# Optimization experiments

Hardware: AMD Instinct MI355X
Metric: run time of the kernel (lower is better)

## Reference

```python
import jax, jax.numpy as jnp
import numpy as np

KH, KW = 3, 3
STRIDE, PAD = 2, 1
NEG_SLOPE = 0.2
EPS = 1e-5


def conv2d(x, w, stride, pad):
    return jax.lax.conv_general_dilated(
        x, w, window_strides=(stride, stride),
        padding=[(pad, pad), (pad, pad)],
        dimension_numbers=('NCHW', 'OIHW', 'NCHW'))


def deform_conv2d(x, offsets, w_def):
    # x: [B,C,H,W]; offsets: [B,2*K,Ho,Wo] (per-kernel-tap (dy,dx) pairs);
    # w_def: [Cout,Cin,KH,KW]. Matches torchvision DeformConv2d (v1, no mask).
    B, C, H, W = x.shape
    Ho, Wo = offsets.shape[2], offsets.shape[3]
    K = KH * KW
    off = offsets.reshape(B, K, 2, Ho, Wo)
    dy, dx = off[:, :, 0], off[:, :, 1]            # [B,K,Ho,Wo]

    ky = jnp.arange(KH).repeat(KW).astype(x.dtype)   # [K]
    kx = jnp.tile(jnp.arange(KW), KH).astype(x.dtype)
    base_y = (jnp.arange(Ho) * STRIDE - PAD).astype(x.dtype)  # [Ho]
    base_x = (jnp.arange(Wo) * STRIDE - PAD).astype(x.dtype)

    # sampling positions [B,K,Ho,Wo]
    py = base_y[None, None, :, None] + ky[None, :, None, None] + dy
    px = base_x[None, None, None, :] + kx[None, :, None, None] + dx

    y0f = jnp.floor(py); x0f = jnp.floor(px)
    wy1 = py - y0f; wy0 = 1.0 - wy1
    wx1 = px - x0f; wx0 = 1.0 - wx1
    y0 = y0f.astype(jnp.int32); x0 = x0f.astype(jnp.int32)
    y1 = y0 + 1; x1 = x0 + 1

    xt = jnp.transpose(x, (0, 2, 3, 1))  # [B,H,W,C] for channel-last gather
    bidx = jnp.arange(B)[:, None, None, None]

    def corner(yi, xi):
        valid = ((yi >= 0) & (yi < H) & (xi >= 0) & (xi < W)).astype(x.dtype)
        yc = jnp.clip(yi, 0, H - 1); xc = jnp.clip(xi, 0, W - 1)
        v = xt[bidx, yc, xc]                         # [B,K,Ho,Wo,C]
        return v * valid[..., None]

    sampled = (corner(y0, x0) * (wy0 * wx0)[..., None]
               + corner(y0, x1) * (wy0 * wx1)[..., None]
               + corner(y1, x0) * (wy1 * wx0)[..., None]
               + corner(y1, x1) * (wy1 * wx1)[..., None])  # [B,K,Ho,Wo,C]

    wk = w_def.reshape(w_def.shape[0], w_def.shape[1], K)   # [Cout,Cin,K]
    return jnp.einsum('bkhwc,ock->bohw', sampled, wk)


def leaky_relu(x):
    return jnp.where(x >= 0, x, NEG_SLOPE * x)


def instance_norm(x):
    mean = jnp.mean(x, axis=(2, 3), keepdims=True)
    var = jnp.var(x, axis=(2, 3), keepdims=True)
    return (x - mean) * jax.lax.rsqrt(var + EPS)


def setup_inputs() -> dict:
    key = jax.random.key(0)
    k1, k2, k3, k4 = jax.random.split(key, 4)
    B, Cin, H, W = 8, 256, 128, 128
    Cout = 256
    x = jax.random.normal(k1, (B, Cin, H, W), dtype=jnp.float32)
    # conv_offset weight: predicts 2*K offset channels
    w_off = jax.random.normal(k2, (2 * KH * KW, Cin, KH, KW), dtype=jnp.float32) * 0.01
    w_def = jax.random.normal(k3, (Cout, Cin, KH, KW), dtype=jnp.float32) * 0.02
    w_1x1 = jax.random.normal(k4, (Cout, Cout, 1, 1), dtype=jnp.float32) * 0.02
    return {"x": x, "w_off": w_off, "w_def": w_def, "w_1x1": w_1x1}


def reference(x, w_off, w_def, w_1x1):
    offsets = conv2d(x, w_off, STRIDE, PAD)          # [B,18,Ho,Wo]
    y = deform_conv2d(x, offsets, w_def)             # [B,Cout,Ho,Wo]
    y = leaky_relu(y)
    y = conv2d(y, w_1x1, 1, 0)
    y = instance_norm(y)
    return leaky_relu(y)
```

## Files before the change

kernel.cpp:

```cpp
#include <hip/hip_runtime.h>

#define B_   8
#define CIN  256
#define H_   128
#define W_   128
#define HO   64
#define WO   64
#define CO_  256
#define NEG  0.2f

typedef __attribute__((ext_vector_type(8))) _Float16 h16x8;
typedef __attribute__((ext_vector_type(4))) float f32x4;
typedef unsigned short u16;

#define OFF_OFS   0
#define WDEF_OFS  589824
#define W1_OFS    884736
#define WBOFF_OFS 917504
#define Y1_OFS    954368
#define XBF_OFS   5148672
#define TAP_OFS   21925888
#define WS_NEED_TAP ((21925888ull + 1179648ull) * 4ull)

__device__ __forceinline__ float lrelu(float v) { return v >= 0.f ? v : NEG * v; }

__device__ __forceinline__ u16 f2h(float f) {
    _Float16 h = (_Float16)f;
    return *(u16*)&h;
}

__device__ __forceinline__ void gld16(const void* g, void* l) {
    __builtin_amdgcn_global_load_lds((const __attribute__((address_space(1))) unsigned*)g,
                                     (__attribute__((address_space(3))) unsigned*)l, 16, 0, 0);
}

__global__ __launch_bounds__(256) void prep(
    const float* __restrict__ wdef, const float* __restrict__ w1,
    const float* __restrict__ woff,
    u16* __restrict__ wdefh, u16* __restrict__ w1h, u16* __restrict__ wboff)
{
    int i = blockIdx.x * 256 + threadIdx.x;
    if (i < 9 * 256 * 256) {
        int c  = i & 255;
        int co = (i >> 8) & 255;
        int k  = i >> 16;
        wdefh[i] = f2h(wdef[((size_t)co * 256 + c) * 9 + k]);
    }
    if (i < 65536) w1h[i] = f2h(w1[i]);
    if (i < 73728) {
        int j  = i & 7;
        int s  = (i >> 3) & 7;
        int co = (i >> 6) & 31;
        int ch = (i >> 11) & 3;
        int k  = i >> 13;
        int c  = ch * 64 + ((s ^ ((co >> 1) & 7)) << 3) + j;
        wboff[i] = (co < 18) ? f2h(woff[((size_t)co * 256 + c) * 9 + k]) : (u16)0;
    }
}

__global__ __launch_bounds__(256) void nchw2nhwc(
    const float* __restrict__ x, u16* __restrict__ xh)
{
    __shared__ float tile[64][128];
    int bid = blockIdx.x;
    int g = bid & 3;
    int y = (bid >> 2) & 127;
    int b = bid >> 9;
    int t = threadIdx.x;

    const float* src = x + ((size_t)(b * 256 + g * 64) * 128 + y) * 128;
#pragma unroll
    for (int p = 0; p < 8; ++p) {
        int i = p * 256 + t;
        int cc = i >> 5, x4 = (i & 31) * 4;
        *(float4*)&tile[cc][x4] = *(const float4*)(src + (size_t)cc * 16384 + x4);
    }
    __syncthreads();

    int xpos = t >> 1, h = t & 1;
    u16 buf[32];
#pragma unroll
    for (int j = 0; j < 32; ++j) buf[j] = f2h(tile[h * 32 + j][xpos]);
    u16* dst = xh + (((size_t)b * 128 + y) * 128 + xpos) * 256 + g * 64 + h * 32;
#pragma unroll
    for (int q = 0; q < 4; ++q)
        *(int4*)(dst + q * 8) = *(int4*)(buf + q * 8);
}

__global__ __launch_bounds__(256) void offconv_mfma(
    const u16* __restrict__ xh, const u16* __restrict__ wboff,
    float* __restrict__ off)
{
    __shared__ __align__(16) char smem[57728];
    u16* xrowU = (u16*)smem;
    u16* bU    = (u16*)(smem + 49536);

    int blk = blockIdx.x;
    blk = (blk & 7) * 64 + (blk >> 3);
    int b = blk >> 6, ho = blk & 63;
    int t = threadIdx.x;
    int lane = t & 63, w = t >> 6;
    int r = lane & 15, kg = lane >> 4;

    const u16* xB = xh + (size_t)b * (128 * 128 * 256);

    f32x4 acc[2];
    acc[0] = f32x4{0.f, 0.f, 0.f, 0.f};
    acc[1] = f32x4{0.f, 0.f, 0.f, 0.f};

    if (t < 24) {
        int ry = t >> 3, s = t & 7;
        *(int4*)(smem + (ry * 129 * 8 + s) * 16) = int4{0, 0, 0, 0};
    }

    for (int ch = 0; ch < 4; ++ch) {
        __syncthreads();
        for (int ry = 0; ry < 3; ++ry) {
            int y = 2 * ho - 1 + ry;
            int rowbase = (ry * 129 + 1) * 128;
            if ((unsigned)y < 128u) {
#pragma unroll
                for (int p = 0; p < 4; ++p) {
                    int u = p * 256 + t;
                    int xpi = u >> 3, s = u & 7;
                    int c8 = s ^ (((xpi + 1) >> 1) & 7);
                    gld16(xB + ((size_t)(y * 128 + xpi)) * 256 + ch * 64 + c8 * 8,
                          smem + rowbase + p * 4096 + w * 1024);
                }
            } else if (ch == 0) {
#pragma unroll
                for (int p = 0; p < 4; ++p)
                    *(int4*)(smem + rowbase + (p * 256 + t) * 16) = int4{0, 0, 0, 0};
            }
        }
        gld16(wboff + (size_t)(0 * 4 + ch) * 2048 + t * 8,
              smem + 49536 + w * 1024);
        __syncthreads();

        for (int k = 0; k < 9; ++k) {
            int buf = k & 1;
            if (k < 8)
                gld16(wboff + (size_t)((k + 1) * 4 + ch) * 2048 + t * 8,
                      smem + 49536 + (buf ^ 1) * 4096 + w * 1024);
            int ky = k / 3, kx = k - 3 * ky;
            int pixA = w * 16 + r;
            int xp = 2 * pixA + kx;
            int abase = (ky * 129 + xp) * 64;
            int swA = (xp >> 1) & 7;
#pragma unroll
            for (int ksub = 0; ksub < 2; ++ksub) {
                int lc = ksub * 4 + kg;
                h16x8 a = *(h16x8*)(xrowU + abase + ((lc ^ swA) << 3));
#pragma unroll
                for (int n = 0; n < 2; ++n) {
                    int co = n * 16 + r;
                    h16x8 bb = *(h16x8*)(bU + buf * 2048 + co * 64 +
                                         ((lc ^ ((co >> 1) & 7)) << 3));
                    acc[n] = __builtin_amdgcn_mfma_f32_16x16x32_f16(a, bb, acc[n], 0, 0, 0);
                }
            }
            __syncthreads();
        }
    }

#pragma unroll
    for (int n = 0; n < 2; ++n) {
        int co = n * 16 + r;
        if (co < 18) {
#pragma unroll
            for (int j = 0; j < 4; ++j) {
                int wo = w * 16 + kg * 4 + j;
                off[(((size_t)b * 18 + co) * 64 + ho) * 64 + wo] = acc[n][j];
            }
        }
    }
}

__global__ __launch_bounds__(256) void tapgen(
    const float* __restrict__ off, int4* __restrict__ tap)
{
    int bid = blockIdx.x;
    int b = bid >> 6, ho = bid & 63;
    for (int i = threadIdx.x; i < 576; i += 256) {
        int pix = i / 9, k = i - 9 * (i / 9);
        int ky = k / 3, kx = k - 3 * ky;
        float dy = off[(((size_t)b * 18 + 2 * k    ) * 64 + ho) * 64 + pix];
        float dx = off[(((size_t)b * 18 + 2 * k + 1) * 64 + ho) * 64 + pix];
        float py = (float)(ho * 2 - 1 + ky) + dy;
        float px = (float)(pix * 2 - 1 + kx) + dx;
        float y0f = floorf(py), x0f = floorf(px);
        int y0 = (int)y0f, x0i = (int)x0f;
        float wy1 = py - y0f, wx1 = px - x0f;
        float wy0 = 1.f - wy1, wx0 = 1.f - wx1;
        int y1i = y0 + 1, x1i = x0i + 1;
        bool vy0 = (unsigned)y0  < 128u;
        bool vy1 = (unsigned)y1i < 128u;
        bool vx0 = (unsigned)x0i < 128u;
        bool vx1 = (unsigned)x1i < 128u;
        int yc0 = min(max(y0, 0), 127), yc1 = min(max(y1i, 0), 127);
        int xc0 = min(max(x0i, 0), 127), xc1 = min(max(x1i, 0), 127);
        int4 e;
        e.x = (yc0 * 128 + xc0) * 512 | (xc1 - xc0) | ((yc1 - yc0) << 1);
        e.y = (int)((unsigned)f2h((vy0 && vx0) ? wy0 * wx0 : 0.f) |
                    ((unsigned)f2h((vy0 && vx1) ? wy0 * wx1 : 0.f) << 16));
        e.z = (int)((unsigned)f2h((vy1 && vx0) ? wy1 * wx0 : 0.f) |
                    ((unsigned)f2h((vy1 && vx1) ? wy1 * wx1 : 0.f) << 16));
        e.w = 0;
        tap[(size_t)bid * 576 + i] = e;
    }
}

__global__ __launch_bounds__(512, 4) void deform_fused(
    const u16* __restrict__ xh, const int4* __restrict__ tap,
    const u16* __restrict__ wdefh, const u16* __restrict__ w1h,
    float* __restrict__ out)
{
    extern __shared__ __align__(16) char smem[];

    int blk = blockIdx.x;
    blk = (blk & 7) * 64 + (blk >> 3);
    int b = blk >> 6, ho = blk & 63;
    int t = threadIdx.x;
    int lane = t & 63, w = t >> 6;
    int r = lane & 15, kg = lane >> 4;
    int pixS = w * 8 + (lane >> 3);
    int cs   = lane & 7;

    f32x4 acc[4][2];
    f32x4 zz = {0.f, 0.f, 0.f, 0.f};
#pragma unroll
    for (int m = 0; m < 4; ++m)
#pragma unroll
        for (int n = 0; n < 2; ++n) acc[m][n] = zz;

    const int4* tapB = tap + (size_t)(b * 64 + ho) * 576 + pixS * 9;
    const char* xb2  = (const char*)(xh + (size_t)b * (128 * 128 * 256)) + cs * 16;

    int sbw = pixS * 128 + ((cs ^ (pixS & 7)) << 4);

    auto stage = [&](int k, int ch, int dbuf) {
        const u16* wk = wdefh + ((size_t)k << 16);
#pragma unroll
        for (int p2 = 0; p2 < 4; ++p2) {
            int i = p2 * 512 + t;
            int co = i >> 3, s = i & 7;
            gld16(wk + (size_t)co * 256 + ch * 64 + ((s ^ (co & 7)) << 3),
                  smem + dbuf * 32768 + p2 * 8192 + w * 1024);
        }
    };

    {
        stage(0, 0, 0);
        int4 e = tapB[0];
        int o00 = e.x & 0x7FFFFE00;
        int dxo = (e.x & 1) << 9;
        int dyo = (e.x & 2) << 15;
        h16x8 c00 = *(const h16x8*)(xb2 + o00);
        h16x8 c01 = *(const h16x8*)(xb2 + o00 + dxo);
        h16x8 c10 = *(const h16x8*)(xb2 + o00 + dyo);
        h16x8 c11 = *(const h16x8*)(xb2 + o00 + dyo + dxo);
        union U { int u; _Float16 h[2]; };
        U u01, u23;
        u01.u = e.y; u23.u = e.z;
        h16x8 v = c00 * u01.h[0] + c01 * u01.h[1] + c10 * u23.h[0] + c11 * u23.h[1];
        *(h16x8*)(smem + 65536 + sbw) = v;
    }
    __syncthreads();

    for (int p = 0; p < 36; ++p) {
        int cur = p & 1;
        bool nx = p < 35;
        int4 e;
        h16x8 c00, c01, c10, c11;
        if (nx) {
            int pn = p + 1;
            int chn = pn / 9, kn = pn - 9 * chn;
            e = tapB[kn];
            int o00 = e.x & 0x7FFFFE00;
            int dxo = (e.x & 1) << 9;
            int dyo = (e.x & 2) << 15;
            const char* base = xb2 + chn * 128;
            c00 = *(const h16x8*)(base + o00);
            c01 = *(const h16x8*)(base + o00 + dxo);
            c10 = *(const h16x8*)(base + o00 + dyo);
            c11 = *(const h16x8*)(base + o00 + dyo + dxo);
            stage(kn, chn, cur ^ 1);
        }
        {
            u16* wb = (u16*)(smem + cur * 32768);
            u16* sb = (u16*)(smem + 65536 + cur * 8192);
            h16x8 af[4], bfr[2];
            __builtin_amdgcn_s_setprio(1);
#pragma unroll
            for (int ksub = 0; ksub < 2; ++ksub) {
                int so = ((ksub * 4 + kg) ^ (r & 7)) << 3;
#pragma unroll
                for (int m = 0; m < 4; ++m)
                    af[m] = *(h16x8*)(sb + (m * 16 + r) * 64 + so);
#pragma unroll
                for (int n = 0; n < 2; ++n)
                    bfr[n] = *(h16x8*)(wb + (w * 32 + n * 16 + r) * 64 + so);
#pragma unroll
                for (int m = 0; m < 4; ++m)
#pragma unroll
                    for (int n = 0; n < 2; ++n)
                        acc[m][n] = __builtin_amdgcn_mfma_f32_16x16x32_f16(af[m], bfr[n], acc[m][n], 0, 0, 0);
            }
            __builtin_amdgcn_s_setprio(0);
        }
        if (nx) {
            union U { int u; _Float16 h[2]; };
            U u01, u23;
            u01.u = e.y; u23.u = e.z;
            h16x8 v = c00 * u01.h[0] + c01 * u01.h[1] + c10 * u23.h[0] + c11 * u23.h[1];
            *(h16x8*)(smem + 65536 + (cur ^ 1) * 8192 + sbw) = v;
        }
        __syncthreads();
    }

    char* outT = smem + 32768;
    int rg = lane >> 4;
#pragma unroll
    for (int m = 0; m < 4; ++m)
#pragma unroll
        for (int n = 0; n < 2; ++n) {
            int co = w * 32 + n * 16 + r;
#pragma unroll
            for (int j = 0; j < 4; ++j) {
                int prow = m * 16 + rg * 4 + j;
                *(u16*)(outT + prow * 512 + ((co * 2) ^ ((prow & 7) << 4))) =
                    f2h(lrelu(acc[m][n][j]));
            }
        }

    auto stage1 = [&](int k2, int dbuf) {
#pragma unroll
        for (int p2 = 0; p2 < 2; ++p2) {
            int i = p2 * 512 + t;
            int o = i >> 2, s = i & 3;
            gld16(w1h + (size_t)o * 256 + k2 * 32 + ((s ^ (o & 3)) << 3),
                  smem + dbuf * 16384 + p2 * 8192 + w * 1024);
        }
    };

    stage1(0, 0);
#pragma unroll
    for (int m = 0; m < 4; ++m)
#pragma unroll
        for (int n = 0; n < 2; ++n) acc[m][n] = zz;
    __syncthreads();

    for (int k2 = 0; k2 < 8; ++k2) {
        int cur = k2 & 1;
        if (k2 < 7) stage1(k2 + 1, cur ^ 1);
        h16x8 af[4], bfr[2];
        __builtin_amdgcn_s_setprio(1);
#pragma unroll
        for (int m = 0; m < 4; ++m) {
            int prow = m * 16 + r;
            af[m] = *(h16x8*)(outT + prow * 512 +
                              ((((k2 << 2) + kg) << 4) ^ ((prow & 7) << 4)));
        }
#pragma unroll
        for (int n = 0; n < 2; ++n) {
            int o = w * 32 + n * 16 + r;
            bfr[n] = *(h16x8*)(smem + cur * 16384 + o * 64 + ((kg ^ (o & 3)) << 4));
        }
#pragma unroll
        for (int m = 0; m < 4; ++m)
#pragma unroll
            for (int n = 0; n < 2; ++n)
                acc[m][n] = __builtin_amdgcn_mfma_f32_16x16x32_f16(af[m], bfr[n], acc[m][n], 0, 0, 0);
        __builtin_amdgcn_s_setprio(0);
        __syncthreads();
    }

#pragma unroll
    for (int m = 0; m < 4; ++m)
#pragma unroll
        for (int n = 0; n < 2; ++n) {
            int o = w * 32 + n * 16 + r;
            int pix0 = m * 16 + rg * 4;
            float4 v;
            v.x = acc[m][n][0]; v.y = acc[m][n][1];
            v.z = acc[m][n][2]; v.w = acc[m][n][3];
            *(float4*)(out + ((size_t)(b * 256 + o) * 64 + ho) * 64 + pix0) = v;
        }
}

__global__ __launch_bounds__(512, 4) void deform_inline(
    const u16* __restrict__ xh, const float* __restrict__ off,
    const u16* __restrict__ wdefh, u16* __restrict__ y1p)
{
    extern __shared__ __align__(16) char smem[];

    int blk = blockIdx.x;
    blk = (blk & 7) * 64 + (blk >> 3);
    int b = blk >> 6, ho = blk & 63;
    int t = threadIdx.x;
    int lane = t & 63, w = t >> 6;
    int r = lane & 15, kg = lane >> 4;
    int pixS = w * 8 + (lane >> 3);
    int cs   = lane & 7;

    f32x4 acc[4][2];
    f32x4 zz = {0.f, 0.f, 0.f, 0.f};
#pragma unroll
    for (int m = 0; m < 4; ++m)
#pragma unroll
        for (int n = 0; n < 2; ++n) acc[m][n] = zz;

    const u16* xB = xh + (size_t)b * (128 * 128 * 256);

    int o00, o01, o10, o11;
    float f00, f01, f10, f11;

    auto coords = [&](int k) {
        int ky = k / 3, kx = k - 3 * ky;
        float dy = off[(((size_t)b * 18 + 2 * k    ) * 64 + ho) * 64 + pixS];
        float dx = off[(((size_t)b * 18 + 2 * k + 1) * 64 + ho) * 64 + pixS];
        float py = (float)(ho * 2 - 1 + ky) + dy;
        float px = (float)(pixS * 2 - 1 + kx) + dx;
        float y0f = floorf(py), x0f = floorf(px);
        int y0 = (int)y0f, x0i = (int)x0f;
        float wy1 = py - y0f, wx1 = px - x0f;
        float wy0 = 1.f - wy1, wx0 = 1.f - wx1;
        int y1i = y0 + 1, x1i = x0i + 1;
        bool vy0 = (unsigned)y0  < 128u;
        bool vy1 = (unsigned)y1i < 128u;
        bool vx0 = (unsigned)x0i < 128u;
        bool vx1 = (unsigned)x1i < 128u;
        int yc0 = min(max(y0, 0), 127), yc1 = min(max(y1i, 0), 127);
        int xc0 = min(max(x0i, 0), 127), xc1 = min(max(x1i, 0), 127);
        o00 = yc0 * 128 + xc0;  o01 = yc0 * 128 + xc1;
        o10 = yc1 * 128 + xc0;  o11 = yc1 * 128 + xc1;
        f00 = (vy0 && vx0) ? wy0 * wx0 : 0.f;
        f01 = (vy0 && vx1) ? wy0 * wx1 : 0.f;
        f10 = (vy1 && vx0) ? wy1 * wx0 : 0.f;
        f11 = (vy1 && vx1) ? wy1 * wx1 : 0.f;
    };

    auto stage = [&](int k, int ch, int dbuf) {
        const u16* wk = wdefh + ((size_t)k << 16);
#pragma unroll
        for (int p2 = 0; p2 < 4; ++p2) {
            int i = p2 * 512 + t;
            int co = i >> 3, s = i & 7;
            gld16(wk + (size_t)co * 256 + ch * 64 + ((s ^ (co & 7)) << 3),
                  smem + dbuf * 32768 + p2 * 8192 + w * 1024);
        }
    };

    auto sample = [&](int ch, int dbuf) {
        int cw = ch * 64 + cs * 8;
        const u16* q00 = xB + (size_t)o00 * 256 + cw;
        const u16* q01 = xB + (size_t)o01 * 256 + cw;
        const u16* q10 = xB + (size_t)o10 * 256 + cw;
        const u16* q11 = xB + (size_t)o11 * 256 + cw;
        h16x8 c00 = *(const h16x8*)q00;
        h16x8 c01 = *(const h16x8*)q01;
        h16x8 c10 = *(const h16x8*)q10;
        h16x8 c11 = *(const h16x8*)q11;
        _Float16 hf00 = (_Float16)f00, hf01 = (_Float16)f01;
        _Float16 hf10 = (_Float16)f10, hf11 = (_Float16)f11;
        h16x8 v = c00 * hf00 + c01 * hf01 + c10 * hf10 + c11 * hf11;
        *(h16x8*)(smem + 65536 + dbuf * 8192 + pixS * 128 + ((cs ^ (pixS & 7)) << 4)) = v;
    };

    coords(0);
    stage(0, 0, 0);
    sample(0, 0);
    __syncthreads();

    for (int p = 0; p < 36; ++p) {
        int cur = p & 1;
        if (p < 35) {
            int pn = p + 1;
            int chn = pn / 9, kn = pn - 9 * chn;
            stage(kn, chn, cur ^ 1);
            coords(kn);
            sample(chn, cur ^ 1);
        }
        u16* wb = (u16*)(smem + cur * 32768);
        u16* sb = (u16*)(smem + 65536 + cur * 8192);
        h16x8 af[4], bfr[2];
        __builtin_amdgcn_s_setprio(1);
#pragma unroll
        for (int ksub = 0; ksub < 2; ++ksub) {
            int so = ((ksub * 4 + kg) ^ (r & 7)) << 3;
#pragma unroll
            for (int m = 0; m < 4; ++m)
                af[m] = *(h16x8*)(sb + (m * 16 + r) * 64 + so);
#pragma unroll
            for (int n = 0; n < 2; ++n)
                bfr[n] = *(h16x8*)(wb + (w * 32 + n * 16 + r) * 64 + so);
#pragma unroll
            for (int m = 0; m < 4; ++m)
#pragma unroll
                for (int n = 0; n < 2; ++n)
                    acc[m][n] = __builtin_amdgcn_mfma_f32_16x16x32_f16(af[m], bfr[n], acc[m][n], 0, 0, 0);
        }
        __builtin_amdgcn_s_setprio(0);
        __syncthreads();
    }

    u16* outT = (u16*)smem;
    int rg = lane >> 4;
#pragma unroll
    for (int m = 0; m < 4; ++m)
#pragma unroll
        for (int n = 0; n < 2; ++n) {
            int co = w * 32 + n * 16 + r;
#pragma unroll
            for (int j = 0; j < 4; ++j) {
                int prow = m * 16 + rg * 4 + j;
                outT[prow * 256 + co] = f2h(lrelu(acc[m][n][j]));
            }
        }
    __syncthreads();
    u16* dst = y1p + (size_t)(b * 64 + ho) * 16384;
#pragma unroll
    for (int p = 0; p < 4; ++p)
        *(int4*)((char*)dst + p * 8192 + t * 16) = *(int4*)(smem + p * 8192 + t * 16);
}

__global__ __launch_bounds__(256) void conv1x1_mfma(
    const u16* __restrict__ y1p, const u16* __restrict__ w1h,
    float* __restrict__ out)
{
    __shared__ __align__(16) char smem[20480];
    u16* btile = (u16*)smem;
    u16* atile = (u16*)(smem + 16384);

    int blk = blockIdx.x;
    blk = (blk & 7) * 64 + (blk >> 3);
    int b = blk >> 6, ho = blk & 63;
    int t = threadIdx.x, lane = t & 63, w = t >> 6;
    int r = lane & 15, kg = lane >> 4;
    int sR = (r >> 1) & 3;

    f32x4 acc[4][4];
    f32x4 zz = {0.f, 0.f, 0.f, 0.f};
#pragma unroll
    for (int m = 0; m < 4; ++m)
#pragma unroll
        for (int n = 0; n < 4; ++n) acc[m][n] = zz;

    const u16* abase = y1p + (size_t)(b * 64 + ho) * 16384;

    for (int ch = 0; ch < 8; ++ch) {
#pragma unroll
        for (int p = 0; p < 4; ++p) {
            int slot = p * 256 + t;
            int o = slot >> 2, qq = slot & 3;
            gld16(w1h + o * 256 + ch * 32 + ((qq ^ ((o >> 1) & 3)) << 3),
                  smem + p * 4096 + (t >> 6) * 1024);
        }
        {
            int pix = t >> 2, qq = t & 3;
            gld16(abase + pix * 256 + ch * 32 + ((qq ^ ((pix >> 1) & 3)) << 3),
                  smem + 16384 + (t >> 6) * 1024);
        }
        __syncthreads();
        h16x8 af[4], bfr[4];
#pragma unroll
        for (int m = 0; m < 4; ++m)
            af[m] = *(h16x8*)(atile + (m * 16 + r) * 32 + ((kg ^ sR) << 3));
#pragma unroll
        for (int n = 0; n < 4; ++n)
            bfr[n] = *(h16x8*)(btile + (w * 64 + n * 16 + r) * 32 + ((kg ^ sR) << 3));
#pragma unroll
        for (int m = 0; m < 4; ++m)
#pragma unroll
            for (int n = 0; n < 4; ++n)
                acc[m][n] = __builtin_amdgcn_mfma_f32_16x16x32_f16(af[m], bfr[n], acc[m][n], 0, 0, 0);
        __syncthreads();
    }

    int rg = lane >> 4;
#pragma unroll
    for (int m = 0; m < 4; ++m)
#pragma unroll
        for (int n = 0; n < 4; ++n) {
            int o = w * 64 + n * 16 + r;
            int pix0 = m * 16 + rg * 4;
            float4 v;
            v.x = acc[m][n][0]; v.y = acc[m][n][1];
            v.z = acc[m][n][2]; v.w = acc[m][n][3];
            *(float4*)(out + ((size_t)(b * 256 + o) * 64 + ho) * 64 + pix0) = v;
        }
}

__global__ __launch_bounds__(256) void instnorm(float* __restrict__ out)
{
    int bc = blockIdx.x;
    float* p = out + (size_t)bc * 4096;
    int t = threadIdx.x;

    float4 v[4];
    float s1 = 0.f, s2 = 0.f;
#pragma unroll
    for (int i = 0; i < 4; ++i) {
        v[i] = *(const float4*)&p[(t + i * 256) * 4];
        s1 += v[i].x + v[i].y + v[i].z + v[i].w;
        s2 += v[i].x * v[i].x + v[i].y * v[i].y + v[i].z * v[i].z + v[i].w * v[i].w;
    }
#pragma unroll
    for (int o = 32; o > 0; o >>= 1) {
        s1 += __shfl_down(s1, o);
        s2 += __shfl_down(s2, o);
    }
    __shared__ float rs[8];
    __shared__ float mb[2];
    int wave = t >> 6;
    if ((t & 63) == 0) { rs[wave] = s1; rs[4 + wave] = s2; }
    __syncthreads();
    if (t == 0) {
        float a = rs[0] + rs[1] + rs[2] + rs[3];
        float qq = rs[4] + rs[5] + rs[6] + rs[7];
        float mean = a * (1.f / 4096.f);
        float var  = qq * (1.f / 4096.f) - mean * mean;
        mb[0] = mean;
        mb[1] = rsqrtf(var + 1e-5f);
    }
    __syncthreads();
    float mean = mb[0], inv = mb[1];
#pragma unroll
    for (int i = 0; i < 4; ++i) {
        float4 u = v[i];
        u.x = lrelu((u.x - mean) * inv);
        u.y = lrelu((u.y - mean) * inv);
        u.z = lrelu((u.z - mean) * inv);
        u.w = lrelu((u.w - mean) * inv);
        *(float4*)&p[(t + i * 256) * 4] = u;
    }
}

extern "C" void kernel_launch(void* const* d_in, const int* in_sizes, int n_in,
                              void* d_out, int out_size, void* d_ws, size_t ws_size,
                              hipStream_t stream)
{
    const float* x     = (const float*)d_in[0];
    const float* w_off = (const float*)d_in[1];
    const float* w_def = (const float*)d_in[2];
    const float* w1    = (const float*)d_in[3];
    float* out = (float*)d_out;
    float* ws  = (float*)d_ws;

    float* off   = ws + OFF_OFS;
    u16*   wdefh = (u16*)(ws + WDEF_OFS);
    u16*   w1h   = (u16*)(ws + W1_OFS);
    u16*   wboff = (u16*)(ws + WBOFF_OFS);
    u16*   y1p   = (u16*)(ws + Y1_OFS);
    u16*   xh    = (u16*)(ws + XBF_OFS);
    int4*  tap   = (int4*)(ws + TAP_OFS);

    const bool use_tap = ws_size >= WS_NEED_TAP;

    hipFuncSetAttribute((const void*)deform_fused,
                        hipFuncAttributeMaxDynamicSharedMemorySize, 81920);
    hipFuncSetAttribute((const void*)deform_inline,
                        hipFuncAttributeMaxDynamicSharedMemorySize, 81920);

    hipLaunchKernelGGL(prep,         dim3(2304), dim3(256), 0, stream, w_def, w1, w_off, wdefh, w1h, wboff);
    hipLaunchKernelGGL(nchw2nhwc,    dim3(4096), dim3(256), 0, stream, x, xh);
    hipLaunchKernelGGL(offconv_mfma, dim3(512),  dim3(256), 0, stream, xh, wboff, off);
    if (use_tap) {
        hipLaunchKernelGGL(tapgen,       dim3(512), dim3(256), 0, stream, off, tap);
        hipLaunchKernelGGL(deform_fused, dim3(512), dim3(512), 81920, stream, xh, tap, wdefh, w1h, out);
    } else {
        hipLaunchKernelGGL(deform_inline, dim3(512), dim3(512), 81920, stream, xh, off, wdefh, y1p);
        hipLaunchKernelGGL(conv1x1_mfma,  dim3(512), dim3(256), 0, stream, y1p, w1h, out);
    }
    hipLaunchKernelGGL(instnorm,     dim3(2048), dim3(256), 0, stream, out);
}
```

Measured before the change: 146.3 us.

## Fuse tap generation into offset conv and restage 1x1 weights single-buffered

Moves the tapgen computation into the tail of offconv_mfma. The offsets are staged in shared memory and the bilinear tap table is written directly, which removes one kernel launch and a global reread of the offsets. Separately, the 1x1-conv stage in deform_fused now loads 64-channel weight chunks into a single buffer, with a sync after each load. This replaces the double-buffered 32-channel prefetch, halving the number of loop iterations but giving up the overlap between weight loads and MFMA work.

```diff
diff --git a/kernel.cpp b/kernel.cpp
--- a/kernel.cpp
+++ b/kernel.cpp
@@ -89,7 +89,7 @@
 
 __global__ __launch_bounds__(256) void offconv_mfma(
     const u16* __restrict__ xh, const u16* __restrict__ wboff,
-    float* __restrict__ off)
+    float* __restrict__ off, int4* __restrict__ tap)
 {
     __shared__ __align__(16) char smem[57728];
     u16* xrowU = (u16*)smem;
@@ -163,6 +163,7 @@
         }
     }
 
+    float* offL = (float*)smem;
 #pragma unroll
     for (int n = 0; n < 2; ++n) {
         int co = n * 16 + r;
@@ -170,43 +171,41 @@
 #pragma unroll
             for (int j = 0; j < 4; ++j) {
                 int wo = w * 16 + kg * 4 + j;
-                off[(((size_t)b * 18 + co) * 64 + ho) * 64 + wo] = acc[n][j];
-            }
-        }
-    }
-}
-
-__global__ __launch_bounds__(256) void tapgen(
-    const float* __restrict__ off, int4* __restrict__ tap)
-{
-    int bid = blockIdx.x;
-    int b = bid >> 6, ho = bid & 63;
-    for (int i = threadIdx.x; i < 576; i += 256) {
-        int pix = i / 9, k = i - 9 * (i / 9);
-        int ky = k / 3, kx = k - 3 * ky;
-        float dy = off[(((size_t)b * 18 + 2 * k    ) * 64 + ho) * 64 + pix];
-        float dx = off[(((size_t)b * 18 + 2 * k + 1) * 64 + ho) * 64 + pix];
-        float py = (float)(ho * 2 - 1 + ky) + dy;
-        float px = (float)(pix * 2 - 1 + kx) + dx;
-        float y0f = floorf(py), x0f = floorf(px);
-        int y0 = (int)y0f, x0i = (int)x0f;
-        float wy1 = py - y0f, wx1 = px - x0f;
-        float wy0 = 1.f - wy1, wx0 = 1.f - wx1;
-        int y1i = y0 + 1, x1i = x0i + 1;
-        bool vy0 = (unsigned)y0  < 128u;
-        bool vy1 = (unsigned)y1i < 128u;
-        bool vx0 = (unsigned)x0i < 128u;
-        bool vx1 = (unsigned)x1i < 128u;
-        int yc0 = min(max(y0, 0), 127), yc1 = min(max(y1i, 0), 127);
-        int xc0 = min(max(x0i, 0), 127), xc1 = min(max(x1i, 0), 127);
-        int4 e;
-        e.x = (yc0 * 128 + xc0) * 512 | (xc1 - xc0) | ((yc1 - yc0) << 1);
-        e.y = (int)((unsigned)f2h((vy0 && vx0) ? wy0 * wx0 : 0.f) |
-                    ((unsigned)f2h((vy0 && vx1) ? wy0 * wx1 : 0.f) << 16));
-        e.z = (int)((unsigned)f2h((vy1 && vx0) ? wy1 * wx0 : 0.f) |
-                    ((unsigned)f2h((vy1 && vx1) ? wy1 * wx1 : 0.f) << 16));
-        e.w = 0;
-        tap[(size_t)bid * 576 + i] = e;
+                float v = acc[n][j];
+                off[(((size_t)b * 18 + co) * 64 + ho) * 64 + wo] = v;
+                offL[co * 64 + wo] = v;
+            }
+        }
+    }
+    if (tap) {
+        __syncthreads();
+        for (int i = t; i < 576; i += 256) {
+            int pix = i / 9, k = i - 9 * (i / 9);
+            int ky = k / 3, kx = k - 3 * ky;
+            float dy = offL[(2 * k) * 64 + pix];
+            float dx = offL[(2 * k + 1) * 64 + pix];
+            float py = (float)(ho * 2 - 1 + ky) + dy;
+            float px = (float)(pix * 2 - 1 + kx) + dx;
+            float y0f = floorf(py), x0f = floorf(px);
+            int y0 = (int)y0f, x0i = (int)x0f;
+            float wy1 = py - y0f, wx1 = px - x0f;
+            float wy0 = 1.f - wy1, wx0 = 1.f - wx1;
+            int y1i = y0 + 1, x1i = x0i + 1;
+            bool vy0 = (unsigned)y0  < 128u;
+            bool vy1 = (unsigned)y1i < 128u;
+            bool vx0 = (unsigned)x0i < 128u;
+            bool vx1 = (unsigned)x1i < 128u;
+            int yc0 = min(max(y0, 0), 127), yc1 = min(max(y1i, 0), 127);
+            int xc0 = min(max(x0i, 0), 127), xc1 = min(max(x1i, 0), 127);
+            int4 e;
+            e.x = (yc0 * 128 + xc0) * 512 | (xc1 - xc0) | ((yc1 - yc0) << 1);
+            e.y = (int)((unsigned)f2h((vy0 && vx0) ? wy0 * wx0 : 0.f) |
+                        ((unsigned)f2h((vy0 && vx1) ? wy0 * wx1 : 0.f) << 16));
+            e.z = (int)((unsigned)f2h((vy1 && vx0) ? wy1 * wx0 : 0.f) |
+                        ((unsigned)f2h((vy1 && vx1) ? wy1 * wx1 : 0.f) << 16));
+            e.w = 0;
+            tap[(size_t)(b * 64 + ho) * 576 + i] = e;
+        }
     }
 }
 
@@ -333,46 +332,51 @@
             }
         }
 
-    auto stage1 = [&](int k2, int dbuf) {
-#pragma unroll
-        for (int p2 = 0; p2 < 2; ++p2) {
+    auto stage1 = [&](int ch2) {
+#pragma unroll
+        for (int p2 = 0; p2 < 4; ++p2) {
             int i = p2 * 512 + t;
-            int o = i >> 2, s = i & 3;
-            gld16(w1h + (size_t)o * 256 + k2 * 32 + ((s ^ (o & 3)) << 3),
-                  smem + dbuf * 16384 + p2 * 8192 + w * 1024);
+            int o = i >> 3, s = i & 7;
+            gld16(w1h + (size_t)o * 256 + ch2 * 64 + ((s ^ (o & 7)) << 3),
+                  smem + p2 * 8192 + w * 1024);
         }
     };
 
-    stage1(0, 0);
+    stage1(0);
 #pragma unroll
     for (int m = 0; m < 4; ++m)
 #pragma unroll
         for (int n = 0; n < 2; ++n) acc[m][n] = zz;
     __syncthreads();
 
-    for (int k2 = 0; k2 < 8; ++k2) {
-        int cur = k2 & 1;
-        if (k2 < 7) stage1(k2 + 1, cur ^ 1);
+    for (int ch2 = 0; ch2 < 4; ++ch2) {
         h16x8 af[4], bfr[2];
         __builtin_amdgcn_s_setprio(1);
 #pragma unroll
-        for (int m = 0; m < 4; ++m) {
-            int prow = m * 16 + r;
-            af[m] = *(h16x8*)(outT + prow * 512 +
-                              ((((k2 << 2) + kg) << 4) ^ ((prow & 7) << 4)));
-        }
-#pragma unroll
-        for (int n = 0; n < 2; ++n) {
-            int o = w * 32 + n * 16 + r;
-            bfr[n] = *(h16x8*)(smem + cur * 16384 + o * 64 + ((kg ^ (o & 3)) << 4));
-        }
-#pragma unroll
-        for (int m = 0; m < 4; ++m)
-#pragma unroll
-            for (int n = 0; n < 2; ++n)
-                acc[m][n] = __builtin_amdgcn_mfma_f32_16x16x32_f16(af[m], bfr[n], acc[m][n], 0, 0, 0);
+        for (int ksub = 0; ksub < 2; ++ksub) {
+            int cb = (ch2 * 64 + (ksub * 4 + kg) * 8) * 2;
+#pragma unroll
+            for (int m = 0; m < 4; ++m) {
+                int prow = m * 16 + r;
+                af[m] = *(h16x8*)(outT + prow * 512 + (cb ^ ((prow & 7) << 4)));
+            }
+#pragma unroll
+            for (int n = 0; n < 2; ++n) {
+                int o = w * 32 + n * 16 + r;
+                bfr[n] = *(h16x8*)(smem + o * 128 + (((ksub * 4 + kg) ^ (o & 7)) << 4));
+            }
+#pragma unroll
+            for (int m = 0; m < 4; ++m)
+#pragma unroll
+                for (int n = 0; n < 2; ++n)
+                    acc[m][n] = __builtin_amdgcn_mfma_f32_16x16x32_f16(af[m], bfr[n], acc[m][n], 0, 0, 0);
+        }
         __builtin_amdgcn_s_setprio(0);
         __syncthreads();
+        if (ch2 < 3) {
+            stage1(ch2 + 1);
+            __syncthreads();
+        }
     }
 
 #pragma unroll
@@ -664,9 +668,9 @@
 
     hipLaunchKernelGGL(prep,         dim3(2304), dim3(256), 0, stream, w_def, w1, w_off, wdefh, w1h, wboff);
     hipLaunchKernelGGL(nchw2nhwc,    dim3(4096), dim3(256), 0, stream, x, xh);
-    hipLaunchKernelGGL(offconv_mfma, dim3(512),  dim3(256), 0, stream, xh, wboff, off);
+    hipLaunchKernelGGL(offconv_mfma, dim3(512),  dim3(256), 0, stream, xh, wboff, off,
+                       use_tap ? tap : (int4*)nullptr);
     if (use_tap) {
-        hipLaunchKernelGGL(tapgen,       dim3(512), dim3(256), 0, stream, off, tap);
         hipLaunchKernelGGL(deform_fused, dim3(512), dim3(512), 81920, stream, xh, tap, wdefh, w1h, out);
     } else {
         hipLaunchKernelGGL(deform_inline, dim3(512), dim3(512), 81920, stream, xh, off, wdefh, y1p);
```

Measured after the change: 144.8 us, median of 2. About the same (-1.0%).
